# Kernel tuning notes

Hardware: AMD Instinct MI355X
Metric: run time of the kernel (lower is better)

Reference implementation:

```python
import jax, jax.numpy as jnp
import numpy as np

# Config (mirrors init_kwargs)
N_PARTS = 4
N_DATASETS = 4
N_VOLUMES = 12
N_TRANSFORMS = 1
TEMP = 0.1
EPS = 1e-6
BS = N_PARTS * N_DATASETS * N_VOLUMES          # 192
N = BS * (N_TRANSFORMS + 1)                    # 384 total rows
PD = N_PARTS * N_DATASETS                      # 16
C, H, W = 32, 48, 48


def setup_inputs() -> dict:
    key = jax.random.key(0)
    k1, k2 = jax.random.split(key)
    reg_pred = jax.random.normal(k1, (N, C, H, W), dtype=jnp.float32)
    mean_representations = jax.random.normal(k2, (N_DATASETS, C, H, W), dtype=jnp.float32)
    return {"reg_pred": reg_pred, "mean_representations": mean_representations}


def reference(reg_pred, mean_representations):
    X = reg_pred.reshape(N, -1)                                  # [N, D]
    ds_id = (jnp.arange(N) // N_PARTS) % N_DATASETS              # dataset id per row
    Mn = mean_representations.reshape(N_DATASETS, -1)[ds_id]     # [N, D] per-row mean
    Z = X - Mn                                                   # demeaned
    # cosine similarity with per-vector norm clamped at eps (torch CosineSimilarity)
    nrm = jnp.maximum(jnp.linalg.norm(Z, axis=1), EPS)
    Zn = Z / nrm[:, None]
    S = (Zn @ Zn.T) / TEMP                                       # [N, N] scaled cos sims
    E = jnp.exp(S)
    # negative (denominator) set for anchor a: all j with j % PD != a % PD
    rem = jnp.arange(N) % PD
    neg_mask = rem[:, None] != rem[None, :]
    Dsum = jnp.sum(E * neg_mask, axis=1)                         # [N]

    p = jnp.arange(BS)
    i1 = p
    i2 = BS + p
    i3 = (p + PD) % N
    i4 = (BS + p + PD) % N

    def pair_loss(a, b):
        # Faithful to original: BOTH terms use the (a,b) numerator similarity
        num = S[a, b]
        en = jnp.exp(num)
        return -(num - jnp.log(en + Dsum[a])) - (num - jnp.log(en + Dsum[b]))

    total = (pair_loss(i1, i2) + pair_loss(i3, i4)
             + pair_loss(i1, i3) + pair_loss(i2, i4)).sum()
    return total / (N_TRANSFORMS * 3 * BS)
```

## Files before the change

### kernel.cpp

```cpp
#include <hip/hip_runtime.h>
#include <hip/hip_bf16.h>
#include <stdint.h>

#define NR 384
#define DD 73728
#define PDV 16
#define BSV 192
#define KSPLIT 128
#define KCH 576
#define BK 32
#define NIT 18
#define RS 40

typedef __bf16 bf16;
typedef __attribute__((ext_vector_type(4))) __bf16 bf16x4;
typedef __attribute__((ext_vector_type(8))) __bf16 bf16x8;
typedef __attribute__((ext_vector_type(4))) float f32x4;

__global__ __launch_bounds__(256, 3) void k_gram(const float* __restrict__ X,
                                                 const float* __restrict__ M,
                                                 float* __restrict__ Gp) {
    __shared__ float msh[4 * KCH];
    __shared__ bf16 ash[2][128 * RS];
    __shared__ bf16 bsh[2][128 * RS];
    const int tid  = threadIdx.x;
    const int lane = tid & 63;
    const int w    = tid >> 6;
    const int quad = lane >> 4;
    const int l15  = lane & 15;
    const int wm   = w & 1, wn = w >> 1;
    const int srow = tid >> 3;
    const int fseg = tid & 7;
    const int mds  = (srow >> 2) & 3;

    int xcd  = blockIdx.x & 7;
    int g    = blockIdx.x >> 3;
    int tile = g % 6;
    int ks   = xcd + 8 * (g / 6);
    int tm = (tile < 3) ? 0 : ((tile < 5) ? 1 : 2);
    int tn = (tile < 3) ? tile : ((tile < 5) ? (tile - 2) : 2);
    const bool diag = (tm == tn);
    const float* Xa = X + (size_t)(tm * 128) * DD;
    const float* Xb = X + (size_t)(tn * 128) * DD;
    size_t k0 = (size_t)ks * KCH;

    for (int i = tid; i < 4 * 144; i += 256) {
        int ds = i / 144;
        int c  = (i - ds * 144) * 4;
        *(float4*)&msh[ds * KCH + c] = *(const float4*)(M + (size_t)ds * DD + k0 + c);
    }

    f32x4 acc[4][4];
#pragma unroll
    for (int i = 0; i < 4; ++i)
#pragma unroll
        for (int j = 0; j < 4; ++j) acc[i][j] = (f32x4){0.f, 0.f, 0.f, 0.f};

    float4 xa[4], xb[4];
    auto load_regs = [&](int it) {
        size_t gk = k0 + (size_t)it * BK + fseg * 4;
#pragma unroll
        for (int p = 0; p < 4; ++p) {
            int row = p * 32 + srow;
            xa[p] = *(const float4*)(Xa + (size_t)row * DD + gk);
            if (!diag) xb[p] = *(const float4*)(Xb + (size_t)row * DD + gk);
        }
    };
    auto write_tiles = [&](int it, int buf) {
        int kc = it * BK + fseg * 4;
        float4 m4 = *(const float4*)&msh[mds * KCH + kc];
#pragma unroll
        for (int p = 0; p < 4; ++p) {
            int row = p * 32 + srow;
            bf16x4 za;
            za[0] = (bf16)(xa[p].x - m4.x); za[1] = (bf16)(xa[p].y - m4.y);
            za[2] = (bf16)(xa[p].z - m4.z); za[3] = (bf16)(xa[p].w - m4.w);
            *(bf16x4*)&ash[buf][row * RS + fseg * 4] = za;
            if (!diag) {
                bf16x4 zb;
                zb[0] = (bf16)(xb[p].x - m4.x); zb[1] = (bf16)(xb[p].y - m4.y);
                zb[2] = (bf16)(xb[p].z - m4.z); zb[3] = (bf16)(xb[p].w - m4.w);
                *(bf16x4*)&bsh[buf][row * RS + fseg * 4] = zb;
            }
        }
    };
    auto compute = [&](int buf) {
        const bf16* bb = diag ? ash[buf] : bsh[buf];
        bf16x8 af[4], bfv[4];
#pragma unroll
        for (int i = 0; i < 4; ++i) {
            int r = wm * 64 + i * 16 + l15;
            af[i] = *(const bf16x8*)&ash[buf][r * RS + quad * 8];
        }
#pragma unroll
        for (int j = 0; j < 4; ++j) {
            int r = wn * 64 + j * 16 + l15;
            bfv[j] = *(const bf16x8*)&bb[r * RS + quad * 8];
        }
#pragma unroll
        for (int i = 0; i < 4; ++i)
#pragma unroll
            for (int j = 0; j < 4; ++j)
                acc[i][j] = __builtin_amdgcn_mfma_f32_16x16x32_bf16(
                    af[i], bfv[j], acc[i][j], 0, 0, 0);
    };

    load_regs(0);
    __syncthreads();
    write_tiles(0, 0);
    load_regs(1);
    __syncthreads();

    for (int it = 0; it < NIT; ++it) {
        int buf = it & 1;
        if (it + 1 < NIT) {
            write_tiles(it + 1, buf ^ 1);
            if (it + 2 < NIT) load_regs(it + 2);
        }
        compute(buf);
        __syncthreads();
    }

    float* gp = Gp + ((size_t)(ks * 6 + tile) << 14);
#pragma unroll
    for (int i = 0; i < 4; ++i) {
        int lr0 = wm * 64 + i * 16 + quad * 4;
#pragma unroll
        for (int j = 0; j < 4; ++j) {
            int lc = wn * 64 + j * 16 + l15;
#pragma unroll
            for (int r = 0; r < 4; ++r)
                gp[(lr0 + r) * 128 + lc] = acc[i][j][r];
        }
    }
}

__global__ __launch_bounds__(256) void k_red(const float* __restrict__ Gp,
                                             float* __restrict__ G,
                                             float* __restrict__ invn,
                                             float* __restrict__ out) {
    int t    = blockIdx.x * 256 + threadIdx.x;
    if (t == 0) out[0] = 0.0f;
    int tile = t >> 14;
    int idx  = t & 16383;
    int lr   = idx >> 7, lc = idx & 127;
    const float* p = Gp + ((size_t)tile << 14) + idx;
    float s = 0.0f;
#pragma unroll 8
    for (int ks = 0; ks < KSPLIT; ++ks) s += p[(size_t)ks * 98304];
    int tm = (tile < 3) ? 0 : ((tile < 5) ? 1 : 2);
    int tn = (tile < 3) ? tile : ((tile < 5) ? (tile - 2) : 2);
    int a = tm * 128 + lr, b = tn * 128 + lc;
    G[(size_t)a * NR + b] = s;
    G[(size_t)b * NR + a] = s;
    if (a == b) invn[a] = 1.0f / fmaxf(sqrtf(s), 1e-6f);
}

__global__ __launch_bounds__(256) void k_dsum(const float* __restrict__ G,
                                              const float* __restrict__ invn,
                                              float* __restrict__ out) {
    const int lane = threadIdx.x & 63;
    const int a    = blockIdx.x * 4 + (threadIdx.x >> 6);
    float ia  = invn[a];
    int arem  = a & 15;
    float acc = 0.0f;
    for (int b = lane; b < NR; b += 64) {
        float s = G[(size_t)a * NR + b] * ia * invn[b] * 10.0f;
        if ((b & 15) != arem) acc += expf(s);
    }
#pragma unroll
    for (int o = 32; o > 0; o >>= 1) acc += __shfl_down(acc, o);
    if (lane == 0) {
        float Dsa = acc;
        int pr[4];
        if (a < 16)       { pr[0] = 192 + a; pr[1] = a + 16;  pr[2] = a + 192; pr[3] = a + 368; }
        else if (a < 192) { pr[0] = 192 + a; pr[1] = a + 16;  pr[2] = a + 192; pr[3] = a - 16; }
        else if (a < 368) { pr[0] = a - 192; pr[1] = a + 16;  pr[2] = a - 192; pr[3] = a - 16; }
        else              { pr[0] = a - 192; pr[1] = a - 368; pr[2] = a - 192; pr[3] = a - 16; }
        float t = 0.0f;
#pragma unroll
        for (int s = 0; s < 4; ++s) {
            int b = pr[s];
            float num = G[(size_t)a * NR + b] * ia * invn[b] * 10.0f;
            t += -num + logf(expf(num) + Dsa);
        }
        atomicAdd(out, t * (1.0f / 576.0f));
    }
}

extern "C" void kernel_launch(void* const* d_in, const int* in_sizes, int n_in,
                              void* d_out, int out_size, void* d_ws, size_t ws_size,
                              hipStream_t stream) {
    const float* X = (const float*)d_in[0];
    const float* M = (const float*)d_in[1];
    float* out = (float*)d_out;

    char* ws = (char*)d_ws;
    float* Gp   = (float*)ws;
    float* G    = Gp + (size_t)KSPLIT * 6 * 16384;
    float* invn = G + (size_t)NR * NR;

    k_gram<<<dim3(6 * KSPLIT), dim3(256), 0, stream>>>(X, M, Gp);
    k_red<<<dim3(384), dim3(256), 0, stream>>>(Gp, G, invn, out);
    k_dsum<<<dim3(NR / 4), dim3(256), 0, stream>>>(G, invn, out);
}
```

Baseline: 194.5 us.

## Precompute demeaned bf16 Z in MFMA-friendly layout, load fragments directly from global

Result: slower. 232.1 us (+19.3%).

```diff
diff --git a/kernel.cpp b/kernel.cpp
--- a/kernel.cpp
+++ b/kernel.cpp
@@ -10,28 +10,48 @@
 #define KCH 576
 #define BK 32
 #define NIT 18
-#define RS 40
+#define KCTOT 2304
+#define ZROW 32
+#define ZKC (NR * ZROW)
 
 typedef __bf16 bf16;
-typedef __attribute__((ext_vector_type(4))) __bf16 bf16x4;
 typedef __attribute__((ext_vector_type(8))) __bf16 bf16x8;
 typedef __attribute__((ext_vector_type(4))) float f32x4;
 
-__global__ __launch_bounds__(256, 3) void k_gram(const float* __restrict__ X,
-                                                 const float* __restrict__ M,
+__global__ __launch_bounds__(256) void k_prep(const float* __restrict__ X,
+                                              const float* __restrict__ M,
+                                              bf16* __restrict__ Zt) {
+    const int r   = blockIdx.x >> 2;
+    const int seg = blockIdx.x & 3;
+    const int ds  = (r >> 2) & 3;
+    const float* xr = X + (size_t)r * DD;
+    const float* mr = M + (size_t)ds * DD;
+    bf16* zr = Zt + (size_t)r * ZROW;
+#pragma unroll 3
+    for (int i = 0; i < 9; ++i) {
+        int c = seg * 2304 + i * 256 + threadIdx.x;
+        int k = c * 8;
+        float4 x0 = *(const float4*)(xr + k);
+        float4 x1 = *(const float4*)(xr + k + 4);
+        float4 m0 = *(const float4*)(mr + k);
+        float4 m1 = *(const float4*)(mr + k + 4);
+        bf16x8 z;
+        z[0] = (bf16)(x0.x - m0.x); z[1] = (bf16)(x0.y - m0.y);
+        z[2] = (bf16)(x0.z - m0.z); z[3] = (bf16)(x0.w - m0.w);
+        z[4] = (bf16)(x1.x - m1.x); z[5] = (bf16)(x1.y - m1.y);
+        z[6] = (bf16)(x1.z - m1.z); z[7] = (bf16)(x1.w - m1.w);
+        *(bf16x8*)(zr + (size_t)(k >> 5) * ZKC + (k & 31)) = z;
+    }
+}
+
+__global__ __launch_bounds__(256, 3) void k_gram(const bf16* __restrict__ Zt,
                                                  float* __restrict__ Gp) {
-    __shared__ float msh[4 * KCH];
-    __shared__ bf16 ash[2][128 * RS];
-    __shared__ bf16 bsh[2][128 * RS];
     const int tid  = threadIdx.x;
     const int lane = tid & 63;
     const int w    = tid >> 6;
     const int quad = lane >> 4;
     const int l15  = lane & 15;
     const int wm   = w & 1, wn = w >> 1;
-    const int srow = tid >> 3;
-    const int fseg = tid & 7;
-    const int mds  = (srow >> 2) & 3;
 
     int xcd  = blockIdx.x & 7;
     int g    = blockIdx.x >> 3;
@@ -39,16 +59,11 @@
     int ks   = xcd + 8 * (g / 6);
     int tm = (tile < 3) ? 0 : ((tile < 5) ? 1 : 2);
     int tn = (tile < 3) ? tile : ((tile < 5) ? (tile - 2) : 2);
-    const bool diag = (tm == tn);
-    const float* Xa = X + (size_t)(tm * 128) * DD;
-    const float* Xb = X + (size_t)(tn * 128) * DD;
-    size_t k0 = (size_t)ks * KCH;
-
-    for (int i = tid; i < 4 * 144; i += 256) {
-        int ds = i / 144;
-        int c  = (i - ds * 144) * 4;
-        *(float4*)&msh[ds * KCH + c] = *(const float4*)(M + (size_t)ds * DD + k0 + c);
-    }
+
+    const bf16* pa = Zt + (size_t)(ks * NIT) * ZKC
+                   + (size_t)(tm * 128 + wm * 64 + l15) * ZROW + quad * 8;
+    const bf16* pb = Zt + (size_t)(ks * NIT) * ZKC
+                   + (size_t)(tn * 128 + wn * 64 + l15) * ZROW + quad * 8;
 
     f32x4 acc[4][4];
 #pragma unroll
@@ -56,69 +71,31 @@
 #pragma unroll
         for (int j = 0; j < 4; ++j) acc[i][j] = (f32x4){0.f, 0.f, 0.f, 0.f};
 
-    float4 xa[4], xb[4];
-    auto load_regs = [&](int it) {
-        size_t gk = k0 + (size_t)it * BK + fseg * 4;
-#pragma unroll
-        for (int p = 0; p < 4; ++p) {
-            int row = p * 32 + srow;
-            xa[p] = *(const float4*)(Xa + (size_t)row * DD + gk);
-            if (!diag) xb[p] = *(const float4*)(Xb + (size_t)row * DD + gk);
-        }
+    bf16x8 a0[4], b0[4], a1[4], b1[4];
+    auto LDF = [&](bf16x8 (&A)[4], bf16x8 (&B)[4], int it) {
+        const bf16* qa = pa + (size_t)it * ZKC;
+        const bf16* qb = pb + (size_t)it * ZKC;
+#pragma unroll
+        for (int i = 0; i < 4; ++i) A[i] = *(const bf16x8*)(qa + i * 512);
+#pragma unroll
+        for (int j = 0; j < 4; ++j) B[j] = *(const bf16x8*)(qb + j * 512);
     };
-    auto write_tiles = [&](int it, int buf) {
-        int kc = it * BK + fseg * 4;
-        float4 m4 = *(const float4*)&msh[mds * KCH + kc];
-#pragma unroll
-        for (int p = 0; p < 4; ++p) {
-            int row = p * 32 + srow;
-            bf16x4 za;
-            za[0] = (bf16)(xa[p].x - m4.x); za[1] = (bf16)(xa[p].y - m4.y);
-            za[2] = (bf16)(xa[p].z - m4.z); za[3] = (bf16)(xa[p].w - m4.w);
-            *(bf16x4*)&ash[buf][row * RS + fseg * 4] = za;
-            if (!diag) {
-                bf16x4 zb;
-                zb[0] = (bf16)(xb[p].x - m4.x); zb[1] = (bf16)(xb[p].y - m4.y);
-                zb[2] = (bf16)(xb[p].z - m4.z); zb[3] = (bf16)(xb[p].w - m4.w);
-                *(bf16x4*)&bsh[buf][row * RS + fseg * 4] = zb;
-            }
-        }
-    };
-    auto compute = [&](int buf) {
-        const bf16* bb = diag ? ash[buf] : bsh[buf];
-        bf16x8 af[4], bfv[4];
-#pragma unroll
-        for (int i = 0; i < 4; ++i) {
-            int r = wm * 64 + i * 16 + l15;
-            af[i] = *(const bf16x8*)&ash[buf][r * RS + quad * 8];
-        }
-#pragma unroll
-        for (int j = 0; j < 4; ++j) {
-            int r = wn * 64 + j * 16 + l15;
-            bfv[j] = *(const bf16x8*)&bb[r * RS + quad * 8];
-        }
+    auto MM = [&](bf16x8 (&A)[4], bf16x8 (&B)[4]) {
 #pragma unroll
         for (int i = 0; i < 4; ++i)
 #pragma unroll
             for (int j = 0; j < 4; ++j)
                 acc[i][j] = __builtin_amdgcn_mfma_f32_16x16x32_bf16(
-                    af[i], bfv[j], acc[i][j], 0, 0, 0);
+                    A[i], B[j], acc[i][j], 0, 0, 0);
     };
 
-    load_regs(0);
-    __syncthreads();
-    write_tiles(0, 0);
-    load_regs(1);
-    __syncthreads();
-
-    for (int it = 0; it < NIT; ++it) {
-        int buf = it & 1;
-        if (it + 1 < NIT) {
-            write_tiles(it + 1, buf ^ 1);
-            if (it + 2 < NIT) load_regs(it + 2);
-        }
-        compute(buf);
-        __syncthreads();
+    LDF(a0, b0, 0);
+#pragma unroll
+    for (int h = 0; h < 9; ++h) {
+        LDF(a1, b1, 2 * h + 1);
+        MM(a0, b0);
+        if (h < 8) LDF(a0, b0, 2 * h + 2);
+        MM(a1, b1);
     }
 
     float* gp = Gp + ((size_t)(ks * 6 + tile) << 14);
@@ -137,10 +114,8 @@
 
 __global__ __launch_bounds__(256) void k_red(const float* __restrict__ Gp,
                                              float* __restrict__ G,
-                                             float* __restrict__ invn,
-                                             float* __restrict__ out) {
+                                             float* __restrict__ invn) {
     int t    = blockIdx.x * 256 + threadIdx.x;
-    if (t == 0) out[0] = 0.0f;
     int tile = t >> 14;
     int idx  = t & 16383;
     int lr   = idx >> 7, lc = idx & 127;
@@ -158,7 +133,7 @@
 
 __global__ __launch_bounds__(256) void k_dsum(const float* __restrict__ G,
                                               const float* __restrict__ invn,
-                                              float* __restrict__ out) {
+                                              float* __restrict__ rt) {
     const int lane = threadIdx.x & 63;
     const int a    = blockIdx.x * 4 + (threadIdx.x >> 6);
     float ia  = invn[a];
@@ -184,8 +159,23 @@
             float num = G[(size_t)a * NR + b] * ia * invn[b] * 10.0f;
             t += -num + logf(expf(num) + Dsa);
         }
-        atomicAdd(out, t * (1.0f / 576.0f));
-    }
+        rt[a] = t;
+    }
+}
+
+__global__ __launch_bounds__(256) void k_fin(const float* __restrict__ rt,
+                                             float* __restrict__ out) {
+    const int tid  = threadIdx.x;
+    const int lane = tid & 63;
+    const int w    = tid >> 6;
+    float s = rt[tid] + ((tid < NR - 256) ? rt[256 + tid] : 0.0f);
+#pragma unroll
+    for (int o = 32; o > 0; o >>= 1) s += __shfl_down(s, o);
+    __shared__ float ps[4];
+    if (lane == 0) ps[w] = s;
+    __syncthreads();
+    if (tid == 0)
+        out[0] = (ps[0] + ps[1] + ps[2] + ps[3]) * (1.0f / 576.0f);
 }
 
 extern "C" void kernel_launch(void* const* d_in, const int* in_sizes, int n_in,
@@ -197,10 +187,14 @@
 
     char* ws = (char*)d_ws;
     float* Gp   = (float*)ws;
-    float* G    = Gp + (size_t)KSPLIT * 6 * 16384;
+    bf16*  Zt   = (bf16*)(ws + (size_t)KSPLIT * 6 * 16384 * 4);
+    float* G    = (float*)((char*)Zt + (size_t)KCTOT * ZKC * 2);
     float* invn = G + (size_t)NR * NR;
-
-    k_gram<<<dim3(6 * KSPLIT), dim3(256), 0, stream>>>(X, M, Gp);
-    k_red<<<dim3(384), dim3(256), 0, stream>>>(Gp, G, invn, out);
-    k_dsum<<<dim3(NR / 4), dim3(256), 0, stream>>>(G, invn, out);
-}
+    float* rt   = invn + NR;
+
+    k_prep<<<dim3(NR * 4), dim3(256), 0, stream>>>(X, M, Zt);
+    k_gram<<<dim3(6 * KSPLIT), dim3(256), 0, stream>>>(Zt, Gp);
+    k_red<<<dim3(384), dim3(256), 0, stream>>>(Gp, G, invn);
+    k_dsum<<<dim3(NR / 4), dim3(256), 0, stream>>>(G, invn, rt);
+    k_fin<<<dim3(1), dim3(256), 0, stream>>>(rt, out);
+}
```

## Fuse split-K reduction with loss tail and write full symmetric partial tiles

Applied to the files above, without the earlier changes.

Measured after the change: 205.1 us. 1.05x slower.

```diff
diff --git a/kernel.cpp b/kernel.cpp
--- a/kernel.cpp
+++ b/kernel.cpp
@@ -5,12 +5,13 @@
 #define NR 384
 #define DD 73728
 #define PDV 16
-#define BSV 192
 #define KSPLIT 128
 #define KCH 576
 #define BK 32
 #define NIT 18
 #define RS 40
+#define TILE_F 16384
+#define KSTRIDE (9 * TILE_F)
 
 typedef __bf16 bf16;
 typedef __attribute__((ext_vector_type(4))) __bf16 bf16x4;
@@ -19,10 +20,14 @@
 
 __global__ __launch_bounds__(256, 3) void k_gram(const float* __restrict__ X,
                                                  const float* __restrict__ M,
-                                                 float* __restrict__ Gp) {
+                                                 float* __restrict__ Gp9,
+                                                 float* __restrict__ Dp,
+                                                 unsigned* __restrict__ ctr) {
     __shared__ float msh[4 * KCH];
-    __shared__ bf16 ash[2][128 * RS];
-    __shared__ bf16 bsh[2][128 * RS];
+    __shared__ __align__(16) char sbuf[41984];
+    bf16* ash = (bf16*)sbuf;
+    bf16* bsh = (bf16*)(sbuf + 20480);
+
     const int tid  = threadIdx.x;
     const int lane = tid & 63;
     const int w    = tid >> 6;
@@ -32,6 +37,8 @@
     const int srow = tid >> 3;
     const int fseg = tid & 7;
     const int mds  = (srow >> 2) & 3;
+
+    if (blockIdx.x == 0 && tid == 0) *ctr = 0u;
 
     int xcd  = blockIdx.x & 7;
     int g    = blockIdx.x >> 3;
@@ -75,22 +82,22 @@
             bf16x4 za;
             za[0] = (bf16)(xa[p].x - m4.x); za[1] = (bf16)(xa[p].y - m4.y);
             za[2] = (bf16)(xa[p].z - m4.z); za[3] = (bf16)(xa[p].w - m4.w);
-            *(bf16x4*)&ash[buf][row * RS + fseg * 4] = za;
+            *(bf16x4*)&ash[buf * 5120 + row * RS + fseg * 4] = za;
             if (!diag) {
                 bf16x4 zb;
                 zb[0] = (bf16)(xb[p].x - m4.x); zb[1] = (bf16)(xb[p].y - m4.y);
                 zb[2] = (bf16)(xb[p].z - m4.z); zb[3] = (bf16)(xb[p].w - m4.w);
-                *(bf16x4*)&bsh[buf][row * RS + fseg * 4] = zb;
+                *(bf16x4*)&bsh[buf * 5120 + row * RS + fseg * 4] = zb;
             }
         }
     };
     auto compute = [&](int buf) {
-        const bf16* bb = diag ? ash[buf] : bsh[buf];
+        const bf16* bb = diag ? (ash + buf * 5120) : (bsh + buf * 5120);
         bf16x8 af[4], bfv[4];
 #pragma unroll
         for (int i = 0; i < 4; ++i) {
             int r = wm * 64 + i * 16 + l15;
-            af[i] = *(const bf16x8*)&ash[buf][r * RS + quad * 8];
+            af[i] = *(const bf16x8*)&ash[buf * 5120 + r * RS + quad * 8];
         }
 #pragma unroll
         for (int j = 0; j < 4; ++j) {
@@ -121,7 +128,7 @@
         __syncthreads();
     }
 
-    float* gp = Gp + ((size_t)(ks * 6 + tile) << 14);
+    float* gp = Gp9 + (size_t)ks * KSTRIDE + (size_t)(tm * 3 + tn) * TILE_F;
 #pragma unroll
     for (int i = 0; i < 4; ++i) {
         int lr0 = wm * 64 + i * 16 + quad * 4;
@@ -133,58 +140,113 @@
                 gp[(lr0 + r) * 128 + lc] = acc[i][j][r];
         }
     }
+
+    if (diag) {
+        if (wm == wn && (l15 >> 2) == quad) {
+#pragma unroll
+            for (int i = 0; i < 4; ++i)
+                Dp[(size_t)ks * NR + tm * 128 + wm * 64 + i * 16 + l15] =
+                    acc[i][i][l15 & 3];
+        }
+    } else {
+        float* tb = (float*)sbuf;
+        float* gpT = Gp9 + (size_t)ks * KSTRIDE + (size_t)(tn * 3 + tm) * TILE_F;
+#pragma unroll
+        for (int h = 0; h < 2; ++h) {
+            __syncthreads();
+            if (wm == h) {
+#pragma unroll
+                for (int i = 0; i < 4; ++i) {
+                    int rr0 = i * 16 + quad * 4;
+#pragma unroll
+                    for (int j = 0; j < 4; ++j) {
+                        int cc = wn * 64 + j * 16 + l15;
+#pragma unroll
+                        for (int r = 0; r < 4; ++r)
+                            tb[(rr0 + r) * 129 + cc] = acc[i][j][r];
+                    }
+                }
+            }
+            __syncthreads();
+#pragma unroll
+            for (int rep = 0; rep < 32; ++rep) {
+                int idx = rep * 256 + tid;
+                int c = idx >> 6;
+                int r = idx & 63;
+                gpT[c * 128 + h * 64 + r] = tb[r * 129 + c];
+            }
+        }
+    }
 }
 
-__global__ __launch_bounds__(256) void k_red(const float* __restrict__ Gp,
-                                             float* __restrict__ G,
-                                             float* __restrict__ invn,
-                                             float* __restrict__ out) {
-    int t    = blockIdx.x * 256 + threadIdx.x;
-    if (t == 0) out[0] = 0.0f;
-    int tile = t >> 14;
-    int idx  = t & 16383;
-    int lr   = idx >> 7, lc = idx & 127;
-    const float* p = Gp + ((size_t)tile << 14) + idx;
-    float s = 0.0f;
+__global__ __launch_bounds__(384) void k_tail(const float* __restrict__ Gp9,
+                                              const float* __restrict__ Dp,
+                                              float* __restrict__ rt,
+                                              unsigned* __restrict__ ctr,
+                                              float* __restrict__ out) {
+    __shared__ float invn_sh[NR];
+    __shared__ float sv[NR];
+    __shared__ float wred[6];
+    __shared__ bool amlast;
+
+    const int tid  = threadIdx.x;
+    const int lane = tid & 63;
+    const int w    = tid >> 6;
+    const int b    = tid;
+    const int a    = blockIdx.x;
+
+    float s2 = 0.f;
+    const float* dp = Dp + b;
 #pragma unroll 8
-    for (int ks = 0; ks < KSPLIT; ++ks) s += p[(size_t)ks * 98304];
-    int tm = (tile < 3) ? 0 : ((tile < 5) ? 1 : 2);
-    int tn = (tile < 3) ? tile : ((tile < 5) ? (tile - 2) : 2);
-    int a = tm * 128 + lr, b = tn * 128 + lc;
-    G[(size_t)a * NR + b] = s;
-    G[(size_t)b * NR + a] = s;
-    if (a == b) invn[a] = 1.0f / fmaxf(sqrtf(s), 1e-6f);
-}
-
-__global__ __launch_bounds__(256) void k_dsum(const float* __restrict__ G,
-                                              const float* __restrict__ invn,
-                                              float* __restrict__ out) {
-    const int lane = threadIdx.x & 63;
-    const int a    = blockIdx.x * 4 + (threadIdx.x >> 6);
-    float ia  = invn[a];
-    int arem  = a & 15;
-    float acc = 0.0f;
-    for (int b = lane; b < NR; b += 64) {
-        float s = G[(size_t)a * NR + b] * ia * invn[b] * 10.0f;
-        if ((b & 15) != arem) acc += expf(s);
-    }
-#pragma unroll
-    for (int o = 32; o > 0; o >>= 1) acc += __shfl_down(acc, o);
-    if (lane == 0) {
-        float Dsa = acc;
+    for (int ks = 0; ks < KSPLIT; ++ks) s2 += dp[(size_t)ks * NR];
+    invn_sh[b] = 1.f / fmaxf(sqrtf(s2), 1e-6f);
+    __syncthreads();
+
+    const int pa = a >> 7, pb = b >> 7;
+    const float* gbase = Gp9 + (size_t)(pa * 3 + pb) * TILE_F
+                       + (size_t)(a & 127) * 128 + (b & 127);
+    float gsum = 0.f;
+#pragma unroll 8
+    for (int ks = 0; ks < KSPLIT; ++ks) gsum += gbase[(size_t)ks * KSTRIDE];
+
+    const float ia = invn_sh[a];
+    const float s  = gsum * ia * invn_sh[b] * 10.0f;
+    sv[b] = s;
+    float e = ((b & 15) != (a & 15)) ? expf(s) : 0.f;
+#pragma unroll
+    for (int o = 32; o > 0; o >>= 1) e += __shfl_down(e, o);
+    if (lane == 0) wred[w] = e;
+    __syncthreads();
+
+    if (tid == 0) {
+        float Dsa = wred[0] + wred[1] + wred[2] + wred[3] + wred[4] + wred[5];
         int pr[4];
         if (a < 16)       { pr[0] = 192 + a; pr[1] = a + 16;  pr[2] = a + 192; pr[3] = a + 368; }
         else if (a < 192) { pr[0] = 192 + a; pr[1] = a + 16;  pr[2] = a + 192; pr[3] = a - 16; }
         else if (a < 368) { pr[0] = a - 192; pr[1] = a + 16;  pr[2] = a - 192; pr[3] = a - 16; }
         else              { pr[0] = a - 192; pr[1] = a - 368; pr[2] = a - 192; pr[3] = a - 16; }
-        float t = 0.0f;
-#pragma unroll
-        for (int s = 0; s < 4; ++s) {
-            int b = pr[s];
-            float num = G[(size_t)a * NR + b] * ia * invn[b] * 10.0f;
+        float t = 0.f;
+#pragma unroll
+        for (int sidx = 0; sidx < 4; ++sidx) {
+            float num = sv[pr[sidx]];
             t += -num + logf(expf(num) + Dsa);
         }
-        atomicAdd(out, t * (1.0f / 576.0f));
+        rt[a] = t;
+        __threadfence();
+        amlast = (atomicAdd(ctr, 1u) == (unsigned)(NR - 1));
+    }
+    __syncthreads();
+
+    if (amlast) {
+        __threadfence();
+        float v = rt[tid];
+#pragma unroll
+        for (int o = 32; o > 0; o >>= 1) v += __shfl_down(v, o);
+        if (lane == 0) wred[w] = v;
+        __syncthreads();
+        if (tid == 0)
+            out[0] = (wred[0] + wred[1] + wred[2] + wred[3] + wred[4] + wred[5])
+                     * (1.0f / 576.0f);
     }
 }
 
@@ -196,11 +258,11 @@
     float* out = (float*)d_out;
 
     char* ws = (char*)d_ws;
-    float* Gp   = (float*)ws;
-    float* G    = Gp + (size_t)KSPLIT * 6 * 16384;
-    float* invn = G + (size_t)NR * NR;
-
-    k_gram<<<dim3(6 * KSPLIT), dim3(256), 0, stream>>>(X, M, Gp);
-    k_red<<<dim3(384), dim3(256), 0, stream>>>(Gp, G, invn, out);
-    k_dsum<<<dim3(NR / 4), dim3(256), 0, stream>>>(G, invn, out);
+    float* Gp9 = (float*)ws;
+    float* Dp  = Gp9 + (size_t)KSPLIT * KSTRIDE;
+    float* rt  = Dp + (size_t)KSPLIT * NR;
+    unsigned* ctr = (unsigned*)(rt + NR);
+
+    k_gram<<<dim3(6 * KSPLIT), dim3(256), 0, stream>>>(X, M, Gp9, Dp, ctr);
+    k_tail<<<dim3(NR), dim3(384), 0, stream>>>(Gp9, Dp, rt, ctr, out);
 }
```
